# Optimization experiments

Hardware: AMD Instinct MI355X
Metric: run time of the kernel (lower is better)

## Reference

```python
import jax, jax.numpy as jnp
import numpy as np

DIM = 128
N_NODES = 100000
N_EDGES = 600000
LN_EPS = 1e-5


def setup_inputs() -> dict:
    key = jax.random.key(0)
    k_x, k_ei, k_ew, k_w, k_b, k_g = jax.random.split(key, 6)
    x = jax.random.normal(k_x, (N_NODES, DIM), dtype=jnp.float32)
    edge_index = jax.random.randint(k_ei, (2, N_EDGES), 0, N_NODES, dtype=jnp.int64)
    edge_weight = jax.random.uniform(k_ew, (N_EDGES,), dtype=jnp.float32, minval=0.05, maxval=1.0)
    # GCNConv linear weight (glorot) + bias; LayerNorm affine params
    limit = float(np.sqrt(6.0 / (DIM + DIM)))
    W = jax.random.uniform(k_w, (DIM, DIM), dtype=jnp.float32, minval=-limit, maxval=limit)
    b = jnp.zeros((DIM,), dtype=jnp.float32)
    gamma = jnp.ones((DIM,), dtype=jnp.float32)
    beta = jnp.zeros((DIM,), dtype=jnp.float32)
    return {"x": x, "edge_index": edge_index, "edge_weight": edge_weight,
            "W": W, "b": b, "gamma": gamma, "beta": beta}


def reference(x, edge_index, edge_weight, W, b, gamma, beta):
    N = x.shape[0]
    row, col = edge_index[0], edge_index[1]  # messages flow row -> col (source_to_target)

    # gcn_norm (add_self_loops=False): deg[j] = sum of incoming edge weights
    deg = jax.ops.segment_sum(edge_weight, col, num_segments=N)
    deg_safe = jnp.where(deg > 0, deg, 1.0)
    dinv = jnp.where(deg > 0, jax.lax.rsqrt(deg_safe), 0.0)
    norm = dinv[row] * edge_weight * dinv[col]  # [E]

    h = x @ W                                   # [N, D] linear transform
    msg = h[row] * norm[:, None]                # gather + scale [E, D]
    agg = jax.ops.segment_sum(msg, col, num_segments=N) + b  # scatter-add [N, D]

    # LayerNorm over feature dim
    mu = jnp.mean(agg, axis=-1, keepdims=True)
    var = jnp.mean((agg - mu) ** 2, axis=-1, keepdims=True)
    ln = (agg - mu) * jax.lax.rsqrt(var + LN_EPS) * gamma + beta

    # GELU (torch default = exact erf form); dropout is identity at eval
    return x + jax.nn.gelu(ln, approximate=False)
```

## Files before the change

kernel.cpp:

```cpp
#include <hip/hip_runtime.h>
#include <hip/hip_fp16.h>
#include <math.h>

#define DIM 128
#define TR 32
#define SA_STRIDE 136

#define DEG_SHIFT 42
#define DEG_SCALE 33554432.0f
#define DEG_MASK ((1ull << DEG_SHIFT) - 1)

typedef __attribute__((ext_vector_type(8))) short bf16x8;
typedef __attribute__((ext_vector_type(4))) float f32x4;

__device__ __forceinline__ ushort f2bf(float f) {
    union { float f; unsigned u; } v; v.f = f;
    unsigned u = v.u;
    return (ushort)((u + 0x7FFFu + ((u >> 16) & 1u)) >> 16);
}

__device__ __forceinline__ ushort f2h(float f) {
    __half h = __float2half_rn(f);
    return *reinterpret_cast<ushort*>(&h);
}

__device__ __forceinline__ float h2f(ushort u) {
    __half_raw hr; hr.x = u;
    return __half2float(__half(hr));
}

__global__ void fill_zero(float* p, int n) {
    int i = blockIdx.x * blockDim.x + threadIdx.x;
    if (i < n) p[i] = 0.f;
}

__global__ void fill_zero4(float4* p, int n4) {
    int i = blockIdx.x * blockDim.x + threadIdx.x;
    if (i < n4) p[i] = make_float4(0.f, 0.f, 0.f, 0.f);
}

__global__ void init_kernel(const float* __restrict__ W, ushort* __restrict__ Wt,
                            const float* __restrict__ x, ushort* __restrict__ xh, int nxh,
                            float* __restrict__ zbase, int nz, int* __restrict__ gctr) {
    int i = blockIdx.x * blockDim.x + threadIdx.x;
    if (i < nxh) {
        const float4* xs = (const float4*)x;
        float4 a = xs[i * 2], c = xs[i * 2 + 1];
        bf16x8 h;
        h[0] = (short)f2h(a.x); h[1] = (short)f2h(a.y);
        h[2] = (short)f2h(a.z); h[3] = (short)f2h(a.w);
        h[4] = (short)f2h(c.x); h[5] = (short)f2h(c.y);
        h[6] = (short)f2h(c.z); h[7] = (short)f2h(c.w);
        *(bf16x8*)&xh[i * 8] = h;
    }
    int j = i - nxh;
    if (j >= 0 && j < 16384) {
        int k = j >> 7, n = j & 127;
        Wt[n * DIM + k] = f2bf(W[k * DIM + n]);
    }
    int z = i - nxh - 16384;
    if (z >= 0 && z < nz) zbase[z] = 0.f;
    if (i == 0) *gctr = 0;
}

__global__ void count_deg_kernel(const int* __restrict__ ei, const float* __restrict__ ew,
                                 unsigned long long* __restrict__ cd,
                                 int* __restrict__ rank, int E) {
    int e = blockIdx.x * blockDim.x + threadIdx.x;
    if (e < E) {
        int col = ei[E + e];
        unsigned long long pk = (1ull << DEG_SHIFT)
                              + (unsigned long long)(ew[e] * DEG_SCALE + 0.5f);
        unsigned long long old = atomicAdd(&cd[col], pk);
        rank[e] = (int)(old >> DEG_SHIFT);
    }
}

__global__ __launch_bounds__(256) void alloc_kernel(const unsigned long long* __restrict__ cd,
                                                    float* __restrict__ dinv,
                                                    int* __restrict__ row_start,
                                                    int* __restrict__ row_end,
                                                    int* __restrict__ gctr, int N) {
    __shared__ int wsum[4];
    __shared__ int sbase;
    int t = threadIdx.x;
    int i = blockIdx.x * 256 + t;
    int lane = t & 63;
    int w = t >> 6;
    unsigned long long p = (i < N) ? cd[i] : 0ull;
    int c = (int)(p >> DEG_SHIFT);
    int pre = c;
#pragma unroll
    for (int off = 1; off < 64; off <<= 1) {
        int v = __shfl_up(pre, off);
        if (lane >= off) pre += v;
    }
    if (lane == 63) wsum[w] = pre;
    __syncthreads();
    if (t == 0) sbase = atomicAdd(gctr, wsum[0] + wsum[1] + wsum[2] + wsum[3]);
    __syncthreads();
    int woff = 0;
#pragma unroll
    for (int k = 0; k < 3; ++k) if (w > k) woff += wsum[k];
    if (i < N) {
        int rs = sbase + woff + pre - c;
        row_start[i] = rs;
        row_end[i] = rs + c;
        float d = (float)(p & DEG_MASK) * (1.0f / DEG_SCALE);
        dinv[i] = d > 0.f ? rsqrtf(d) : 0.f;
    }
}

__global__ void csr_fill_kernel(const int* __restrict__ ei, const float* __restrict__ ew,
                                const int* __restrict__ rank,
                                const int* __restrict__ row_start,
                                const float* __restrict__ dinv,
                                int2* __restrict__ csr, int E) {
    int e = blockIdx.x * blockDim.x + threadIdx.x;
    if (e < E) {
        int row = ei[e];
        int col = ei[E + e];
        int p = row_start[col] + rank[e];
        float w = dinv[row] * ew[e];
        csr[p] = make_int2(row, __float_as_int(w));
    }
}

template<bool XH>
__global__ __launch_bounds__(256) void gather_mfma_ln_kernel(
        const int2* __restrict__ csr, const int* __restrict__ row_start,
        const int* __restrict__ seg_end, const float* __restrict__ dinv,
        const float* __restrict__ x, const ushort* __restrict__ xh,
        const ushort* __restrict__ Wt, const float* __restrict__ b,
        const float* __restrict__ gamma, const float* __restrict__ beta,
        float* __restrict__ out, int N) {
    __shared__ ushort sA[TR * SA_STRIDE];
    __shared__ float redS[4][16];
    __shared__ float redQ[4][16];

    const int tid  = threadIdx.x;
    const int l32  = tid & 31;
    const int g32  = tid >> 5;
    const int lane = tid & 63;
    const int w    = tid >> 6;
    const int row0 = blockIdx.x * TR;

    const float4* xv = (const float4*)x;
    const ushort4* xhv = (const ushort4*)xh;
    int sidx[4], eidx[4];
    float dv[4];
    float4 accq[4];
    int maxlen = 0;
#pragma unroll
    for (int q = 0; q < 4; ++q) {
        int node = row0 + g32 * 4 + q;
        int ok = node < N;
        sidx[q] = ok ? row_start[node] : 0;
        eidx[q] = ok ? seg_end[node] : 0;
        dv[q]   = ok ? dinv[node] : 0.f;
        accq[q] = make_float4(0.f, 0.f, 0.f, 0.f);
        int len = eidx[q] - sidx[q];
        maxlen = len > maxlen ? len : maxlen;
    }
#pragma unroll 2
    for (int it = 0; it < maxlen; ++it) {
        int2 pk[4];
#pragma unroll
        for (int q = 0; q < 4; ++q) {
            int j = sidx[q] + it;
            pk[q] = csr[j < eidx[q] ? j : 0];
        }
#pragma unroll
        for (int q = 0; q < 4; ++q) {
            float wt = (sidx[q] + it < eidx[q]) ? __int_as_float(pk[q].y) : 0.f;
            float4 v;
            if (XH) {
                ushort4 hv = xhv[(size_t)pk[q].x * 32 + l32];
                v = make_float4(h2f(hv.x), h2f(hv.y), h2f(hv.z), h2f(hv.w));
            } else {
                v = xv[(size_t)pk[q].x * 32 + l32];
            }
            accq[q].x += wt * v.x; accq[q].y += wt * v.y;
            accq[q].z += wt * v.z; accq[q].w += wt * v.w;
        }
    }
#pragma unroll
    for (int q = 0; q < 4; ++q) {
        int r = g32 * 4 + q;
        ushort4 p4;
        p4.x = f2bf(accq[q].x * dv[q]); p4.y = f2bf(accq[q].y * dv[q]);
        p4.z = f2bf(accq[q].z * dv[q]); p4.w = f2bf(accq[q].w * dv[q]);
        *(ushort4*)&sA[r * SA_STRIDE + l32 * 4] = p4;
    }
    __syncthreads();

    const int m16  = lane & 15;
    const int quad = lane >> 4;
    const int tm   = w & 1;
    const int tnb  = (w >> 1) * 4;

    bf16x8 afrag[4];
    const ushort* arow = &sA[(16 * tm + m16) * SA_STRIDE + quad * 8];
#pragma unroll
    for (int kb = 0; kb < 4; ++kb)
        afrag[kb] = *(const bf16x8*)(arow + kb * 32);

    f32x4 acc[4];
#pragma unroll
    for (int t = 0; t < 4; ++t) { acc[t][0] = 0.f; acc[t][1] = 0.f; acc[t][2] = 0.f; acc[t][3] = 0.f; }

#pragma unroll
    for (int kb = 0; kb < 4; ++kb) {
#pragma unroll
        for (int t = 0; t < 4; ++t) {
            const ushort* bp = Wt + (size_t)((tnb + t) * 16 + m16) * DIM + kb * 32 + quad * 8;
            bf16x8 bfrag = *(const bf16x8*)bp;
            acc[t] = __builtin_amdgcn_mfma_f32_16x16x32_bf16(afrag[kb], bfrag, acc[t], 0, 0, 0);
        }
    }

    float gcol[4], becol[4];
#pragma unroll
    for (int t = 0; t < 4; ++t) {
        int col = (tnb + t) * 16 + m16;
        float bc = b[col];
        gcol[t]  = gamma[col];
        becol[t] = beta[col];
#pragma unroll
        for (int i = 0; i < 4; ++i) acc[t][i] += bc;
    }

    float s[4], sq[4];
#pragma unroll
    for (int i = 0; i < 4; ++i) {
        s[i]  = acc[0][i] + acc[1][i] + acc[2][i] + acc[3][i];
        sq[i] = acc[0][i]*acc[0][i] + acc[1][i]*acc[1][i] + acc[2][i]*acc[2][i] + acc[3][i]*acc[3][i];
    }
#pragma unroll
    for (int off = 1; off <= 8; off <<= 1) {
#pragma unroll
        for (int i = 0; i < 4; ++i) {
            s[i]  += __shfl_xor(s[i], off);
            sq[i] += __shfl_xor(sq[i], off);
        }
    }
    if (m16 == 0) {
#pragma unroll
        for (int i = 0; i < 4; ++i) {
            redS[w][quad * 4 + i] = s[i];
            redQ[w][quad * 4 + i] = sq[i];
        }
    }
    __syncthreads();

#pragma unroll
    for (int i = 0; i < 4; ++i) {
        int rloc = quad * 4 + i;
        float tot  = redS[w][rloc] + redS[w ^ 2][rloc];
        float totq = redQ[w][rloc] + redQ[w ^ 2][rloc];
        float mu   = tot * (1.0f / DIM);
        float var  = totq * (1.0f / DIM) - mu * mu;
        float rstd = rsqrtf(var + 1e-5f);
        int r = row0 + 16 * tm + rloc;
        if (r < N) {
#pragma unroll
            for (int t = 0; t < 4; ++t) {
                int col = (tnb + t) * 16 + m16;
                float l = (acc[t][i] - mu) * rstd * gcol[t] + becol[t];
                float g = 0.5f * l * (1.0f + erff(l * 0.70710678118654752f));
                out[(size_t)r * DIM + col] = x[(size_t)r * DIM + col] + g;
            }
        }
    }
}

__global__ void deg_kernel(const int* __restrict__ ei, const float* __restrict__ ew,
                           float* __restrict__ deg, int E) {
    int e = blockIdx.x * blockDim.x + threadIdx.x;
    if (e < E) atomicAdd(&deg[ei[E + e]], ew[e]);
}

__global__ void dinv_kernel(float* deg, int N) {
    int i = blockIdx.x * blockDim.x + threadIdx.x;
    if (i < N) {
        float d = deg[i];
        deg[i] = d > 0.f ? rsqrtf(d) : 0.f;
    }
}

__global__ void scatter_kernel(const int* __restrict__ ei, const float* __restrict__ ew,
                               const float* __restrict__ dinv, const float* __restrict__ x,
                               float* __restrict__ out, int E) {
    int t = blockIdx.x * blockDim.x + threadIdx.x;
    int e = t >> 5;
    if (e >= E) return;
    int lane = t & 31;
    int row = ei[e];
    int col = ei[E + e];
    float w = dinv[row] * ew[e] * dinv[col];
    float4 v = *(const float4*)(x + (size_t)row * DIM + (lane << 2));
    float* dst = out + (size_t)col * DIM + (lane << 2);
    atomicAdd(dst + 0, v.x * w);
    atomicAdd(dst + 1, v.y * w);
    atomicAdd(dst + 2, v.z * w);
    atomicAdd(dst + 3, v.w * w);
}

__global__ __launch_bounds__(256) void gemm_ln_kernel(const float* __restrict__ x,
                                                      const float* __restrict__ W,
                                                      const float* __restrict__ b,
                                                      const float* __restrict__ gamma,
                                                      const float* __restrict__ beta,
                                                      float* __restrict__ out, int N) {
    __shared__ float sT[DIM][TR + 4];
    const int tid = threadIdx.x;
    const int row0 = blockIdx.x * TR;
    {
        int r = tid >> 3;
        int c0 = (tid & 7) << 4;
        int rr = row0 + r; if (rr > N - 1) rr = N - 1;
        const float4* src = (const float4*)(out + (size_t)rr * DIM + c0);
#pragma unroll
        for (int i = 0; i < 4; ++i) {
            float4 v = src[i];
            int c = c0 + i * 4;
            sT[c + 0][r] = v.x; sT[c + 1][r] = v.y; sT[c + 2][r] = v.z; sT[c + 3][r] = v.w;
        }
    }
    __syncthreads();
    const int tx = tid & 31;
    const int ty = tid >> 5;
    float acc[4][4] = {};
    const float4* Wv = (const float4*)W;
#pragma unroll 4
    for (int k = 0; k < DIM; ++k) {
        float4 wv = Wv[k * 32 + tx];
        float4 a  = *(const float4*)(&sT[k][ty * 4]);
        acc[0][0] += a.x * wv.x; acc[0][1] += a.x * wv.y; acc[0][2] += a.x * wv.z; acc[0][3] += a.x * wv.w;
        acc[1][0] += a.y * wv.x; acc[1][1] += a.y * wv.y; acc[1][2] += a.y * wv.z; acc[1][3] += a.y * wv.w;
        acc[2][0] += a.z * wv.x; acc[2][1] += a.z * wv.y; acc[2][2] += a.z * wv.z; acc[2][3] += a.z * wv.w;
        acc[3][0] += a.w * wv.x; acc[3][1] += a.w * wv.y; acc[3][2] += a.w * wv.z; acc[3][3] += a.w * wv.w;
    }
    float4 b4 = ((const float4*)b)[tx];
#pragma unroll
    for (int i = 0; i < 4; ++i) {
        acc[i][0] += b4.x; acc[i][1] += b4.y; acc[i][2] += b4.z; acc[i][3] += b4.w;
    }
    float4 g4  = ((const float4*)gamma)[tx];
    float4 be4 = ((const float4*)beta)[tx];
#pragma unroll
    for (int i = 0; i < 4; ++i) {
        float s  = acc[i][0] + acc[i][1] + acc[i][2] + acc[i][3];
        float sq = acc[i][0]*acc[i][0] + acc[i][1]*acc[i][1] + acc[i][2]*acc[i][2] + acc[i][3]*acc[i][3];
#pragma unroll
        for (int off = 16; off > 0; off >>= 1) {
            s  += __shfl_xor(s, off);
            sq += __shfl_xor(sq, off);
        }
        float mu   = s * (1.0f / DIM);
        float var  = sq * (1.0f / DIM) - mu * mu;
        float rstd = rsqrtf(var + 1e-5f);
        int r = row0 + ty * 4 + i;
        if (r < N) {
            float4 xr = *(const float4*)(x + (size_t)r * DIM + tx * 4);
            float lg[4] = {g4.x, g4.y, g4.z, g4.w};
            float lb[4] = {be4.x, be4.y, be4.z, be4.w};
            float lx[4] = {xr.x, xr.y, xr.z, xr.w};
            float o[4];
#pragma unroll
            for (int c = 0; c < 4; ++c) {
                float l = (acc[i][c] - mu) * rstd * lg[c] + lb[c];
                float g = 0.5f * l * (1.0f + erff(l * 0.70710678118654752f));
                o[c] = lx[c] + g;
            }
            *(float4*)(out + (size_t)r * DIM + tx * 4) = make_float4(o[0], o[1], o[2], o[3]);
        }
    }
}

extern "C" void kernel_launch(void* const* d_in, const int* in_sizes, int n_in,
                              void* d_out, int out_size, void* d_ws, size_t ws_size,
                              hipStream_t stream) {
    const float* x     = (const float*)d_in[0];
    const int*   ei    = (const int*)d_in[1];
    const float* ew    = (const float*)d_in[2];
    const float* W     = (const float*)d_in[3];
    const float* b     = (const float*)d_in[4];
    const float* gamma = (const float*)d_in[5];
    const float* beta  = (const float*)d_in[6];
    const int N = in_sizes[0] / DIM;
    const int E = in_sizes[2];
    float* out = (float*)d_out;

    const int nb = (N + 255) / 256;

    size_t hdr_words = 8192 + (size_t)5 * N + (size_t)E + 1;
    hdr_words = (hdr_words + 3) & ~(size_t)3;
    size_t xh_words = (size_t)N * (DIM / 2);
    size_t need_basic = (hdr_words + (size_t)2 * E) * sizeof(float);
    size_t need_xh    = (hdr_words + xh_words + (size_t)2 * E) * sizeof(float);

    if (ws_size >= need_basic) {
        const bool use_xh = (ws_size >= need_xh);
        ushort* Wt         = (ushort*)d_ws;
        unsigned long long* cd = (unsigned long long*)((float*)d_ws + 8192);
        float*  dinv       = (float*)d_ws + 8192 + (size_t)2 * N;
        int*    row_start  = (int*)(dinv + N);
        int*    row_end    = row_start + N;
        int*    rank       = row_end + N;
        int*    gctr       = rank + E;
        ushort* xh         = (ushort*)((float*)d_ws + hdr_words);
        int2*   csr        = (int2*)((float*)d_ws + hdr_words + (use_xh ? xh_words : 0));

        int nxh = use_xh ? N * (DIM / 8) : 0;
        int initn = nxh + 16384 + 2 * N;
        init_kernel<<<(initn + 255) / 256, 256, 0, stream>>>(W, Wt, x, xh, nxh,
                                                             (float*)cd, 2 * N, gctr);
        count_deg_kernel<<<(E + 255) / 256, 256, 0, stream>>>(ei, ew, cd, rank, E);
        alloc_kernel<<<nb, 256, 0, stream>>>(cd, dinv, row_start, row_end, gctr, N);
        csr_fill_kernel<<<(E + 255) / 256, 256, 0, stream>>>(ei, ew, rank, row_start, dinv, csr, E);

        if (use_xh) {
            gather_mfma_ln_kernel<true><<<(N + TR - 1) / TR, 256, 0, stream>>>(
                csr, row_start, row_end, dinv, x, xh, Wt, b, gamma, beta, out, N);
        } else {
            gather_mfma_ln_kernel<false><<<(N + TR - 1) / TR, 256, 0, stream>>>(
                csr, row_start, row_end, dinv, x, xh, Wt, b, gamma, beta, out, N);
        }
    } else {
        float* deg = (float*)d_ws;
        int n4 = N * DIM / 4;
        fill_zero4<<<(n4 + 255) / 256, 256, 0, stream>>>((float4*)out, n4);
        fill_zero<<<nb, 256, 0, stream>>>(deg, N);
        deg_kernel<<<(E + 255) / 256, 256, 0, stream>>>(ei, ew, deg, E);
        dinv_kernel<<<nb, 256, 0, stream>>>(deg, N);
        long long sthreads = (long long)E * 32;
        scatter_kernel<<<(int)((sthreads + 255) / 256), 256, 0, stream>>>(ei, ew, deg, x, out, E);
        gemm_ln_kernel<<<(N + TR - 1) / TR, 256, 0, stream>>>(x, W, b, gamma, beta, out, N);
    }
}
```

Before: 239.0 us.

## Widen fp16 gather to 16-byte loads and overlap x conversion with degree atomics

The fp16 gather path now has 16 lanes per node, each loading 8 halves (16 bytes) per neighbour, with 2 nodes per thread group instead of 4. Wider loads should cut instruction count and improve memory-level parallelism per row fetch. The x-to-fp16 conversion also moves out of the init kernel into the degree-counting kernel, so its streaming work can hide the latency of the atomics. The cost is more registers for the 8-wide accumulators and a more complex count kernel.

```diff
diff --git a/kernel.cpp b/kernel.cpp
--- a/kernel.cpp
+++ b/kernel.cpp
@@ -10,7 +10,7 @@
 #define DEG_SCALE 33554432.0f
 #define DEG_MASK ((1ull << DEG_SHIFT) - 1)
 
-typedef __attribute__((ext_vector_type(8))) short bf16x8;
+typedef __attribute__((ext_vector_type(8))) short s16x8;
 typedef __attribute__((ext_vector_type(4))) float f32x4;
 
 __device__ __forceinline__ ushort f2bf(float f) {
@@ -40,40 +40,43 @@
 }
 
 __global__ void init_kernel(const float* __restrict__ W, ushort* __restrict__ Wt,
-                            const float* __restrict__ x, ushort* __restrict__ xh, int nxh,
                             float* __restrict__ zbase, int nz, int* __restrict__ gctr) {
     int i = blockIdx.x * blockDim.x + threadIdx.x;
-    if (i < nxh) {
-        const float4* xs = (const float4*)x;
+    if (i < 16384) {
+        int k = i >> 7, n = i & 127;
+        Wt[n * DIM + k] = f2bf(W[k * DIM + n]);
+    }
+    int z = i - 16384;
+    if (z >= 0 && z < nz) zbase[z] = 0.f;
+    if (i == 0) *gctr = 0;
+}
+
+__global__ void count_deg_kernel(const int* __restrict__ ei, const float* __restrict__ ew,
+                                 unsigned long long* __restrict__ cd,
+                                 int* __restrict__ rank,
+                                 const float* __restrict__ x, ushort* __restrict__ xh,
+                                 int nxh, int E) {
+    int e = blockIdx.x * blockDim.x + threadIdx.x;
+    int nthreads = gridDim.x * blockDim.x;
+    unsigned long long old = 0;
+    bool valid = (e < E);
+    if (valid) {
+        int col = ei[E + e];
+        unsigned long long pk = (1ull << DEG_SHIFT)
+                              + (unsigned long long)(ew[e] * DEG_SCALE + 0.5f);
+        old = atomicAdd(&cd[col], pk);
+    }
+    const float4* xs = (const float4*)x;
+    for (int i = e; i < nxh; i += nthreads) {
         float4 a = xs[i * 2], c = xs[i * 2 + 1];
-        bf16x8 h;
+        s16x8 h;
         h[0] = (short)f2h(a.x); h[1] = (short)f2h(a.y);
         h[2] = (short)f2h(a.z); h[3] = (short)f2h(a.w);
         h[4] = (short)f2h(c.x); h[5] = (short)f2h(c.y);
         h[6] = (short)f2h(c.z); h[7] = (short)f2h(c.w);
-        *(bf16x8*)&xh[i * 8] = h;
-    }
-    int j = i - nxh;
-    if (j >= 0 && j < 16384) {
-        int k = j >> 7, n = j & 127;
-        Wt[n * DIM + k] = f2bf(W[k * DIM + n]);
-    }
-    int z = i - nxh - 16384;
-    if (z >= 0 && z < nz) zbase[z] = 0.f;
-    if (i == 0) *gctr = 0;
-}
-
-__global__ void count_deg_kernel(const int* __restrict__ ei, const float* __restrict__ ew,
-                                 unsigned long long* __restrict__ cd,
-                                 int* __restrict__ rank, int E) {
-    int e = blockIdx.x * blockDim.x + threadIdx.x;
-    if (e < E) {
-        int col = ei[E + e];
-        unsigned long long pk = (1ull << DEG_SHIFT)
-                              + (unsigned long long)(ew[e] * DEG_SCALE + 0.5f);
-        unsigned long long old = atomicAdd(&cd[col], pk);
-        rank[e] = (int)(old >> DEG_SHIFT);
-    }
+        *(s16x8*)&xh[i * 8] = h;
+    }
+    if (valid) rank[e] = (int)(old >> DEG_SHIFT);
 }
 
 __global__ __launch_bounds__(256) void alloc_kernel(const unsigned long long* __restrict__ cd,
@@ -139,58 +142,98 @@
     __shared__ float redQ[4][16];
 
     const int tid  = threadIdx.x;
-    const int l32  = tid & 31;
-    const int g32  = tid >> 5;
     const int lane = tid & 63;
     const int w    = tid >> 6;
     const int row0 = blockIdx.x * TR;
 
-    const float4* xv = (const float4*)x;
-    const ushort4* xhv = (const ushort4*)xh;
-    int sidx[4], eidx[4];
-    float dv[4];
-    float4 accq[4];
-    int maxlen = 0;
-#pragma unroll
-    for (int q = 0; q < 4; ++q) {
-        int node = row0 + g32 * 4 + q;
-        int ok = node < N;
-        sidx[q] = ok ? row_start[node] : 0;
-        eidx[q] = ok ? seg_end[node] : 0;
-        dv[q]   = ok ? dinv[node] : 0.f;
-        accq[q] = make_float4(0.f, 0.f, 0.f, 0.f);
-        int len = eidx[q] - sidx[q];
-        maxlen = len > maxlen ? len : maxlen;
-    }
+    if (XH) {
+        const int l16 = tid & 15;
+        const int g16 = tid >> 4;
+        const s16x8* xh8 = (const s16x8*)xh;
+        int sidx[2], eidx[2];
+        float dv[2];
+        float accq[2][8];
+        int maxlen = 0;
+#pragma unroll
+        for (int q = 0; q < 2; ++q) {
+            int node = row0 + g16 * 2 + q;
+            int ok = node < N;
+            sidx[q] = ok ? row_start[node] : 0;
+            eidx[q] = ok ? seg_end[node] : 0;
+            dv[q]   = ok ? dinv[node] : 0.f;
+#pragma unroll
+            for (int e8 = 0; e8 < 8; ++e8) accq[q][e8] = 0.f;
+            int len = eidx[q] - sidx[q];
+            maxlen = len > maxlen ? len : maxlen;
+        }
 #pragma unroll 2
-    for (int it = 0; it < maxlen; ++it) {
-        int2 pk[4];
+        for (int it = 0; it < maxlen; ++it) {
+            int2 pk[2];
+#pragma unroll
+            for (int q = 0; q < 2; ++q) {
+                int j = sidx[q] + it;
+                pk[q] = csr[j < eidx[q] ? j : 0];
+            }
+#pragma unroll
+            for (int q = 0; q < 2; ++q) {
+                float wt = (sidx[q] + it < eidx[q]) ? __int_as_float(pk[q].y) : 0.f;
+                s16x8 hv = xh8[(size_t)pk[q].x * 16 + l16];
+#pragma unroll
+                for (int e8 = 0; e8 < 8; ++e8)
+                    accq[q][e8] += wt * h2f((ushort)hv[e8]);
+            }
+        }
+#pragma unroll
+        for (int q = 0; q < 2; ++q) {
+            int r = g16 * 2 + q;
+            s16x8 p8;
+#pragma unroll
+            for (int e8 = 0; e8 < 8; ++e8) p8[e8] = (short)f2bf(accq[q][e8] * dv[q]);
+            *(s16x8*)&sA[r * SA_STRIDE + l16 * 8] = p8;
+        }
+    } else {
+        const int l32 = tid & 31;
+        const int g32 = tid >> 5;
+        const float4* xv = (const float4*)x;
+        int sidx[4], eidx[4];
+        float dv[4];
+        float4 accq[4];
+        int maxlen = 0;
 #pragma unroll
         for (int q = 0; q < 4; ++q) {
-            int j = sidx[q] + it;
-            pk[q] = csr[j < eidx[q] ? j : 0];
+            int node = row0 + g32 * 4 + q;
+            int ok = node < N;
+            sidx[q] = ok ? row_start[node] : 0;
+            eidx[q] = ok ? seg_end[node] : 0;
+            dv[q]   = ok ? dinv[node] : 0.f;
+            accq[q] = make_float4(0.f, 0.f, 0.f, 0.f);
+            int len = eidx[q] - sidx[q];
+            maxlen = len > maxlen ? len : maxlen;
+        }
+#pragma unroll 2
+        for (int it = 0; it < maxlen; ++it) {
+            int2 pk[4];
+#pragma unroll
+            for (int q = 0; q < 4; ++q) {
+                int j = sidx[q] + it;
+                pk[q] = csr[j < eidx[q] ? j : 0];
+            }
+#pragma unroll
+            for (int q = 0; q < 4; ++q) {
+                float wt = (sidx[q] + it < eidx[q]) ? __int_as_float(pk[q].y) : 0.f;
+                float4 v = xv[(size_t)pk[q].x * 32 + l32];
+                accq[q].x += wt * v.x; accq[q].y += wt * v.y;
+                accq[q].z += wt * v.z; accq[q].w += wt * v.w;
+            }
         }
 #pragma unroll
         for (int q = 0; q < 4; ++q) {
-            float wt = (sidx[q] + it < eidx[q]) ? __int_as_float(pk[q].y) : 0.f;
-            float4 v;
-            if (XH) {
-                ushort4 hv = xhv[(size_t)pk[q].x * 32 + l32];
-                v = make_float4(h2f(hv.x), h2f(hv.y), h2f(hv.z), h2f(hv.w));
-            } else {
-                v = xv[(size_t)pk[q].x * 32 + l32];
-            }
-            accq[q].x += wt * v.x; accq[q].y += wt * v.y;
-            accq[q].z += wt * v.z; accq[q].w += wt * v.w;
-        }
-    }
-#pragma unroll
-    for (int q = 0; q < 4; ++q) {
-        int r = g32 * 4 + q;
-        ushort4 p4;
-        p4.x = f2bf(accq[q].x * dv[q]); p4.y = f2bf(accq[q].y * dv[q]);
-        p4.z = f2bf(accq[q].z * dv[q]); p4.w = f2bf(accq[q].w * dv[q]);
-        *(ushort4*)&sA[r * SA_STRIDE + l32 * 4] = p4;
+            int r = g32 * 4 + q;
+            ushort4 p4;
+            p4.x = f2bf(accq[q].x * dv[q]); p4.y = f2bf(accq[q].y * dv[q]);
+            p4.z = f2bf(accq[q].z * dv[q]); p4.w = f2bf(accq[q].w * dv[q]);
+            *(ushort4*)&sA[r * SA_STRIDE + l32 * 4] = p4;
+        }
     }
     __syncthreads();
 
@@ -199,11 +242,11 @@
     const int tm   = w & 1;
     const int tnb  = (w >> 1) * 4;
 
-    bf16x8 afrag[4];
+    s16x8 afrag[4];
     const ushort* arow = &sA[(16 * tm + m16) * SA_STRIDE + quad * 8];
 #pragma unroll
     for (int kb = 0; kb < 4; ++kb)
-        afrag[kb] = *(const bf16x8*)(arow + kb * 32);
+        afrag[kb] = *(const s16x8*)(arow + kb * 32);
 
     f32x4 acc[4];
 #pragma unroll
@@ -214,7 +257,7 @@
 #pragma unroll
         for (int t = 0; t < 4; ++t) {
             const ushort* bp = Wt + (size_t)((tnb + t) * 16 + m16) * DIM + kb * 32 + quad * 8;
-            bf16x8 bfrag = *(const bf16x8*)bp;
+            s16x8 bfrag = *(const s16x8*)bp;
             acc[t] = __builtin_amdgcn_mfma_f32_16x16x32_bf16(afrag[kb], bfrag, acc[t], 0, 0, 0);
         }
     }
@@ -413,10 +456,9 @@
         int2*   csr        = (int2*)((float*)d_ws + hdr_words + (use_xh ? xh_words : 0));
 
         int nxh = use_xh ? N * (DIM / 8) : 0;
-        int initn = nxh + 16384 + 2 * N;
-        init_kernel<<<(initn + 255) / 256, 256, 0, stream>>>(W, Wt, x, xh, nxh,
-                                                             (float*)cd, 2 * N, gctr);
-        count_deg_kernel<<<(E + 255) / 256, 256, 0, stream>>>(ei, ew, cd, rank, E);
+        int initn = 16384 + 2 * N;
+        init_kernel<<<(initn + 255) / 256, 256, 0, stream>>>(W, Wt, (float*)cd, 2 * N, gctr);
+        count_deg_kernel<<<(E + 255) / 256, 256, 0, stream>>>(ei, ew, cd, rank, x, xh, nxh, E);
         alloc_kernel<<<nb, 256, 0, stream>>>(cd, dinv, row_start, row_end, gctr, N);
         csr_fill_kernel<<<(E + 255) / 256, 256, 0, stream>>>(ei, ew, rank, row_start, dinv, csr, E);
 
```

Result: faster. 231.5 us (-3.1%).
